# Kernel tuning notes

Measured on AMD Instinct MI355X. Metric: run time of the kernel, lower is better.

The kernel has to match this reference:

```python
import jax, jax.numpy as jnp
import numpy as np

B, N, C = 64, 1024, 128


def setup_inputs() -> dict:
    key = jax.random.key(0)
    k1, k2, k3, k4, k5, k6 = jax.random.split(key, 6)
    adj_vals = jax.random.uniform(k1, (B, N, N), dtype=jnp.float32)
    mask = jax.random.uniform(k2, (B, N, N)) < 0.1
    adjacent = jnp.where(mask, adj_vals, 0.0)
    annotations = jax.random.normal(k3, (B, N, C), dtype=jnp.float32)
    # GraphConvolution bias, shape (1,1,C)
    gc_bias = jax.random.normal(k4, (1, 1, C), dtype=jnp.float32) * 0.05
    # Keras GRU params (reset_after=True default): kernel (C,3C), recurrent (C,3C), bias (2,3C)
    kernel = jax.random.normal(k5, (C, 3 * C), dtype=jnp.float32) / np.sqrt(C)
    recurrent_kernel = jax.random.normal(k6, (C, 3 * C), dtype=jnp.float32) / np.sqrt(C)
    gru_bias = jnp.zeros((2, 3 * C), dtype=jnp.float32)
    return {"adjacent": adjacent, "annotations": annotations, "gc_bias": gc_bias,
            "kernel": kernel, "recurrent_kernel": recurrent_kernel, "gru_bias": gru_bias}


def reference(adjacent, annotations, gc_bias, kernel, recurrent_kernel, gru_bias):
    # GraphConvolution: per-graph adj @ annotations, batched, + bias
    v = jnp.einsum('bij,bjc->bic', adjacent, annotations) + gc_bias  # [B,N,C]
    b, n, c = v.shape
    x = v.reshape(-1, c)            # visible states, one GRU step each
    h = annotations.reshape(-1, c)  # initial hidden states
    # single-step Keras GRU (reset_after=True)
    mx = x @ kernel + gru_bias[0]
    mh = h @ recurrent_kernel + gru_bias[1]
    xz, xr, xh = jnp.split(mx, 3, axis=-1)
    hz, hr, hh_in = jnp.split(mh, 3, axis=-1)
    z = jax.nn.sigmoid(xz + hz)
    r = jax.nn.sigmoid(xr + hr)
    hh = jnp.tanh(xh + r * hh_in)
    out = z * h + (1.0 - z) * hh
    return out.reshape(b, n, c)
```

## Files before the change

### kernel.cpp

```cpp
#include <hip/hip_runtime.h>

typedef unsigned short ushort_t;
typedef __attribute__((ext_vector_type(8))) short bf16x8;
typedef __attribute__((ext_vector_type(8))) unsigned short u16x8;
typedef __attribute__((ext_vector_type(4))) float f32x4;

#define B_ 64
#define N_ 1024
#define C_ 128

static __device__ __forceinline__ float bf2f(unsigned short u) {
  union { unsigned int i; float f; } v; v.i = ((unsigned int)u) << 16; return v.f;
}
static __device__ __forceinline__ unsigned short f2bf(float f) {
  union { float f; unsigned int i; } v; v.f = f;
  unsigned int i = v.i;
  return (unsigned short)((i + 0x7FFFu + ((i >> 16) & 1u)) >> 16);
}
static __device__ __forceinline__ void split1(float x, ushort_t& h, ushort_t& l) {
  union { float f; unsigned int i; } u; u.f = x;
  h = (ushort_t)(u.i >> 16);
  union { unsigned int i; float f; } t; t.i = u.i & 0xFFFF0000u;
  union { float f; unsigned int i; } w; w.f = x - t.f;
  l = (ushort_t)(w.i >> 16);
}
static __device__ __forceinline__ bf16x8 as_bf(u16x8 v) {
  union { u16x8 u; bf16x8 b; } x; x.u = v; return x.b;
}
static __device__ __forceinline__ void gload_lds16(const void* g, void* l) {
  __builtin_amdgcn_global_load_lds((const __attribute__((address_space(1))) void*)g,
                                   (__attribute__((address_space(3))) void*)l,
                                   16, 0, 0);
}

__global__ __launch_bounds__(256) void tsplit(const float* __restrict__ src,
                                              ushort_t* __restrict__ dh,
                                              ushort_t* __restrict__ dl,
                                              int rows, int cols, long sb, long db) {
  __shared__ float tile[64][65];
  const int t = threadIdx.x;
  src += (long)blockIdx.z * sb;
  dh  += (long)blockIdx.z * db;
  dl  += (long)blockIdx.z * db;
  const int r0 = blockIdx.y * 64, c0 = blockIdx.x * 64;
#pragma unroll
  for (int p = 0; p < 4; ++p) {
    int row = p * 16 + (t >> 4), c4 = (t & 15) * 4;
    f32x4 v = *(const f32x4*)(src + (long)(r0 + row) * cols + c0 + c4);
#pragma unroll
    for (int j = 0; j < 4; ++j) tile[row][c4 + j] = v[j];
  }
  __syncthreads();
  const int oc = t >> 2;
#pragma unroll
  for (int p = 0; p < 2; ++p) {
    int ck = (t & 3) + p * 4;
    u16x8 vh, vl;
#pragma unroll
    for (int j = 0; j < 8; ++j) {
      ushort_t hj, lj;
      split1(tile[ck * 8 + j][oc], hj, lj);
      vh[j] = hj; vl[j] = lj;
    }
    long o = (long)(c0 + oc) * rows + r0 + ck * 8;
    *(u16x8*)(dh + o) = vh;
    *(u16x8*)(dl + o) = vl;
  }
}

__global__ __launch_bounds__(256, 2) void gc_gemm(const float* __restrict__ adj,
                                                  const ushort_t* __restrict__ annTh,
                                                  const ushort_t* __restrict__ annTl,
                                                  const float* __restrict__ gcb,
                                                  float* __restrict__ vout) {
  __shared__ __align__(16) ushort_t ldsAh[128 * 64];
  __shared__ __align__(16) ushort_t ldsAl[128 * 64];
  __shared__ __align__(16) ushort_t ldsBh[128 * 64];
  __shared__ __align__(16) ushort_t ldsBl[128 * 64];
  const int tid = threadIdx.x;
  const int w = tid >> 6, lane = tid & 63;
  const int wr = w >> 1, wc = w & 1;
  const int b = blockIdx.x >> 3;
  const int m0 = (blockIdx.x & 7) * 128;

  const float*    adjb = adj   + ((long)b * N_ + m0) * N_;
  const ushort_t* aThb = annTh + (long)b * C_ * N_;
  const ushort_t* aTlb = annTl + (long)b * C_ * N_;

  const int srow8 = lane >> 3;
  const int klog  = ((lane & 7) * 16) ^ (srow8 << 4);
  const int fr = lane & 15;
  const int kg = lane >> 4;

  f32x4 acc[4][4] = {};

  for (int k0 = 0; k0 < N_; k0 += 64) {
#pragma unroll
    for (int jj = 0; jj < 4; ++jj) {
      int j = w * 4 + jj;
      long so = (long)(j * 8 + srow8) * N_ + k0 + (klog >> 1);
      gload_lds16(aThb + so, (void*)&ldsBh[j * 512]);
      gload_lds16(aTlb + so, (void*)&ldsBl[j * 512]);
    }
#pragma unroll
    for (int q = 0; q < 4; ++q) {
      int ch = q * 256 + tid;
      int row = ch >> 3, ce = ch & 7;
      const float* g = adjb + (long)row * N_ + k0 + ce * 8;
      f32x4 a0 = *(const f32x4*)g;
      f32x4 a1 = *(const f32x4*)(g + 4);
      u16x8 vh, vl;
#pragma unroll
      for (int j = 0; j < 4; ++j) {
        ushort_t hj, lj;
        split1(a0[j], hj, lj); vh[j] = hj; vl[j] = lj;
        split1(a1[j], hj, lj); vh[4 + j] = hj; vl[4 + j] = lj;
      }
      int kb = (ce * 16) ^ ((row & 7) << 4);
      *(u16x8*)((char*)ldsAh + row * 128 + kb) = vh;
      *(u16x8*)((char*)ldsAl + row * 128 + kb) = vl;
    }
    __syncthreads();
#pragma unroll
    for (int kk = 0; kk < 2; ++kk) {
      bf16x8 ah[4], al[4], bh[4], bl[4];
#pragma unroll
      for (int mi = 0; mi < 4; ++mi) {
        int row = wr * 64 + mi * 16 + fr;
        int kb = (kk * 64 + kg * 16) ^ ((row & 7) << 4);
        ah[mi] = *(const bf16x8*)((const char*)ldsAh + row * 128 + kb);
        al[mi] = *(const bf16x8*)((const char*)ldsAl + row * 128 + kb);
      }
#pragma unroll
      for (int ni = 0; ni < 4; ++ni) {
        int row = wc * 64 + ni * 16 + fr;
        int kb = (kk * 64 + kg * 16) ^ ((row & 7) << 4);
        bh[ni] = *(const bf16x8*)((const char*)ldsBh + row * 128 + kb);
        bl[ni] = *(const bf16x8*)((const char*)ldsBl + row * 128 + kb);
      }
#pragma unroll
      for (int mi = 0; mi < 4; ++mi)
#pragma unroll
        for (int ni = 0; ni < 4; ++ni) {
          acc[mi][ni] = __builtin_amdgcn_mfma_f32_16x16x32_bf16(ah[mi], bh[ni], acc[mi][ni], 0, 0, 0);
          acc[mi][ni] = __builtin_amdgcn_mfma_f32_16x16x32_bf16(al[mi], bh[ni], acc[mi][ni], 0, 0, 0);
          acc[mi][ni] = __builtin_amdgcn_mfma_f32_16x16x32_bf16(ah[mi], bl[ni], acc[mi][ni], 0, 0, 0);
        }
    }
    __syncthreads();
  }

  const long rowbase = (long)b * N_ + m0 + wr * 64;
#pragma unroll
  for (int ni = 0; ni < 4; ++ni) {
    int col = wc * 64 + ni * 16 + fr;
    float bias = gcb[col];
#pragma unroll
    for (int mi = 0; mi < 4; ++mi)
#pragma unroll
      for (int r = 0; r < 4; ++r)
        vout[(rowbase + mi * 16 + kg * 4 + r) * C_ + col] = acc[mi][ni][r] + bias;
  }
}

#define GATE(G, AK0, AK1, AR0, AR1)                                                         \
  do {                                                                                      \
    const ushort_t* kh_ = kTh + (long)((G) * C_ + cb) * C_;                                 \
    const ushort_t* kl_ = kTl + (long)((G) * C_ + cb) * C_;                                 \
    const ushort_t* rh_ = rTh + (long)((G) * C_ + cb) * C_;                                 \
    bf16x8 KH[4], KL[4], RH[4];                                                             \
    _Pragma("unroll")                                                                       \
    for (int kk = 0; kk < 4; ++kk) {                                                        \
      int o_ = kk * 32 + kg * 8;                                                            \
      KH[kk] = *(const bf16x8*)(kh_ + o_);                                                  \
      KL[kk] = *(const bf16x8*)(kl_ + o_);                                                  \
      RH[kk] = *(const bf16x8*)(rh_ + o_);                                                  \
    }                                                                                       \
    _Pragma("unroll")                                                                       \
    for (int kk = 0; kk < 4; ++kk) {                                                        \
      AK0 = __builtin_amdgcn_mfma_f32_16x16x32_bf16(xh[0][kk], KH[kk], AK0, 0, 0, 0);       \
      AK1 = __builtin_amdgcn_mfma_f32_16x16x32_bf16(xh[1][kk], KH[kk], AK1, 0, 0, 0);       \
      AK0 = __builtin_amdgcn_mfma_f32_16x16x32_bf16(xl[0][kk], KH[kk], AK0, 0, 0, 0);       \
      AK1 = __builtin_amdgcn_mfma_f32_16x16x32_bf16(xl[1][kk], KH[kk], AK1, 0, 0, 0);       \
      AK0 = __builtin_amdgcn_mfma_f32_16x16x32_bf16(xh[0][kk], KL[kk], AK0, 0, 0, 0);       \
      AK1 = __builtin_amdgcn_mfma_f32_16x16x32_bf16(xh[1][kk], KL[kk], AK1, 0, 0, 0);       \
    }                                                                                       \
    _Pragma("unroll")                                                                       \
    for (int kk = 0; kk < 4; ++kk) {                                                        \
      AR0 = __builtin_amdgcn_mfma_f32_16x16x32_bf16(hh[0][kk], RH[kk], AR0, 0, 0, 0);       \
      AR1 = __builtin_amdgcn_mfma_f32_16x16x32_bf16(hh[1][kk], RH[kk], AR1, 0, 0, 0);       \
    }                                                                                       \
  } while (0)

__global__ __launch_bounds__(256, 2) void gru(const float* __restrict__ v,
                                              const float* __restrict__ ann,
                                              const ushort_t* __restrict__ kTh,
                                              const ushort_t* __restrict__ kTl,
                                              const ushort_t* __restrict__ rTh,
                                              const float* __restrict__ gb,
                                              float* __restrict__ out) {
  const int w = threadIdx.x >> 6, lane = threadIdx.x & 63;
  const long m0 = ((long)blockIdx.x * 4 + w) * 32;
  const int fr = lane & 15, kg = lane >> 4;

  bf16x8 xh[2][4], xl[2][4], hh[2][4];
#pragma unroll
  for (int s = 0; s < 2; ++s)
#pragma unroll
    for (int kk = 0; kk < 4; ++kk) {
      long off = (m0 + s * 16 + fr) * (long)C_ + kk * 32 + kg * 8;
      f32x4 x0 = *(const f32x4*)(v + off);
      f32x4 x1 = *(const f32x4*)(v + off + 4);
      u16x8 th, tl;
#pragma unroll
      for (int j = 0; j < 4; ++j) {
        ushort_t hj, lj;
        split1(x0[j], hj, lj); th[j] = hj; tl[j] = lj;
        split1(x1[j], hj, lj); th[4 + j] = hj; tl[4 + j] = lj;
      }
      xh[s][kk] = as_bf(th); xl[s][kk] = as_bf(tl);
      f32x4 h0 = *(const f32x4*)(ann + off);
      f32x4 h1 = *(const f32x4*)(ann + off + 4);
      u16x8 hv;
#pragma unroll
      for (int j = 0; j < 4; ++j) { hv[j] = f2bf(h0[j]); hv[4 + j] = f2bf(h1[j]); }
      hh[s][kk] = as_bf(hv);
    }

#pragma unroll 1
  for (int n = 0; n < 8; ++n) {
    const int cb = n * 16 + fr;
    f32x4 az0 = {}, az1 = {}, ar0 = {}, ar1 = {}, ax0 = {}, ax1 = {}, ah0 = {}, ah1 = {};
    GATE(0, az0, az1, az0, az1);
    GATE(1, ar0, ar1, ar0, ar1);
    GATE(2, ax0, ax1, ah0, ah1);

    const float bz  = gb[cb] + gb[384 + cb];
    const float brr = gb[128 + cb] + gb[384 + 128 + cb];
    const float bxh = gb[256 + cb];
    const float bhi = gb[384 + 256 + cb];
#pragma unroll
    for (int s = 0; s < 2; ++s) {
      const f32x4& az_ = s ? az1 : az0;
      const f32x4& ar_ = s ? ar1 : ar0;
      const f32x4& ax_ = s ? ax1 : ax0;
      const f32x4& ah_ = s ? ah1 : ah0;
#pragma unroll
      for (int r = 0; r < 4; ++r) {
        long row = m0 + s * 16 + kg * 4 + r;
        float hval = ann[row * C_ + cb];
        float zz = 1.f / (1.f + __expf(-(az_[r] + bz)));
        float rr = 1.f / (1.f + __expf(-(ar_[r] + brr)));
        float hpre = ax_[r] + bxh + rr * (ah_[r] + bhi);
        hpre = fminf(fmaxf(hpre, -15.f), 15.f);
        float e2 = __expf(2.f * hpre);
        float th = (e2 - 1.f) / (e2 + 1.f);
        out[row * C_ + cb] = zz * hval + (1.f - zz) * th;
      }
    }
  }
}

extern "C" void kernel_launch(void* const* d_in, const int* in_sizes, int n_in,
                              void* d_out, int out_size, void* d_ws, size_t ws_size,
                              hipStream_t stream) {
  const float* adj = (const float*)d_in[0];
  const float* ann = (const float*)d_in[1];
  const float* gcb = (const float*)d_in[2];
  const float* ker = (const float*)d_in[3];
  const float* rk  = (const float*)d_in[4];
  const float* gb  = (const float*)d_in[5];
  float* out = (float*)d_out;

  char* ws = (char*)d_ws;
  ushort_t* annTh = (ushort_t*)(ws);
  ushort_t* annTl = (ushort_t*)(ws + 16777216);
  ushort_t* kTh   = (ushort_t*)(ws + 33554432);
  ushort_t* kTl   = (ushort_t*)(ws + 33652736);
  ushort_t* rTh   = (ushort_t*)(ws + 33751040);
  ushort_t* rTl   = (ushort_t*)(ws + 33849344);
  float*    v     = (float*)(ws + 33947648);

  hipLaunchKernelGGL(tsplit, dim3(2, 16, 64), dim3(256), 0, stream,
                     ann, annTh, annTl, 1024, 128, (long)1024 * 128, (long)128 * 1024);
  hipLaunchKernelGGL(tsplit, dim3(6, 2, 1), dim3(256), 0, stream,
                     ker, kTh, kTl, 128, 384, 0L, 0L);
  hipLaunchKernelGGL(tsplit, dim3(6, 2, 1), dim3(256), 0, stream,
                     rk, rTh, rTl, 128, 384, 0L, 0L);
  hipLaunchKernelGGL(gc_gemm, dim3(512), dim3(256), 0, stream, adj, annTh, annTl, gcb, v);
  hipLaunchKernelGGL(gru, dim3(512), dim3(256), 0, stream, v, ann, kTh, kTl, rTh, gb, out);
}
```

Baseline: 198.9 us.

## Fuse graph-conv GEMM and GRU into one kernel via LDS staging

After: 165.0 us. 1.21x faster.

```diff
diff --git a/kernel.cpp b/kernel.cpp
--- a/kernel.cpp
+++ b/kernel.cpp
@@ -9,9 +9,6 @@
 #define N_ 1024
 #define C_ 128
 
-static __device__ __forceinline__ float bf2f(unsigned short u) {
-  union { unsigned int i; float f; } v; v.i = ((unsigned int)u) << 16; return v.f;
-}
 static __device__ __forceinline__ unsigned short f2bf(float f) {
   union { float f; unsigned int i; } v; v.f = f;
   unsigned int i = v.i;
@@ -68,20 +65,28 @@
   }
 }
 
-__global__ __launch_bounds__(256, 2) void gc_gemm(const float* __restrict__ adj,
-                                                  const ushort_t* __restrict__ annTh,
-                                                  const ushort_t* __restrict__ annTl,
-                                                  const float* __restrict__ gcb,
-                                                  float* __restrict__ vout) {
-  __shared__ __align__(16) ushort_t ldsAh[128 * 64];
-  __shared__ __align__(16) ushort_t ldsAl[128 * 64];
-  __shared__ __align__(16) ushort_t ldsBh[128 * 64];
-  __shared__ __align__(16) ushort_t ldsBl[128 * 64];
+__global__ __launch_bounds__(256, 2) void gc_gru(const float* __restrict__ adj,
+                                                 const ushort_t* __restrict__ annTh,
+                                                 const ushort_t* __restrict__ annTl,
+                                                 const float* __restrict__ ann,
+                                                 const float* __restrict__ gcb,
+                                                 const ushort_t* __restrict__ kTh,
+                                                 const ushort_t* __restrict__ kTl,
+                                                 const ushort_t* __restrict__ rTh,
+                                                 const float* __restrict__ gb,
+                                                 float* __restrict__ out) {
+  __shared__ __align__(16) float vlds[128 * 132];
+  ushort_t* ldsAh = (ushort_t*)vlds;
+  ushort_t* ldsAl = ldsAh + 128 * 64;
+  ushort_t* ldsBh = ldsAl + 128 * 64;
+  ushort_t* ldsBl = ldsBh + 128 * 64;
+
   const int tid = threadIdx.x;
   const int w = tid >> 6, lane = tid & 63;
   const int wr = w >> 1, wc = w & 1;
-  const int b = blockIdx.x >> 3;
-  const int m0 = (blockIdx.x & 7) * 128;
+  const int swz = (blockIdx.x & 7) * 64 + (blockIdx.x >> 3);
+  const int b = swz >> 3;
+  const int m0 = (swz & 7) * 128;
 
   const float*    adjb = adj   + ((long)b * N_ + m0) * N_;
   const ushort_t* aThb = annTh + (long)b * C_ * N_;
@@ -150,18 +155,47 @@
     __syncthreads();
   }
 
-  const long rowbase = (long)b * N_ + m0 + wr * 64;
 #pragma unroll
   for (int ni = 0; ni < 4; ++ni) {
     int col = wc * 64 + ni * 16 + fr;
     float bias = gcb[col];
 #pragma unroll
-    for (int mi = 0; mi < 4; ++mi)
+    for (int mi = 0; mi < 4; ++mi) {
+      int row = wr * 64 + mi * 16 + kg * 4;
 #pragma unroll
       for (int r = 0; r < 4; ++r)
-        vout[(rowbase + mi * 16 + kg * 4 + r) * C_ + col] = acc[mi][ni][r] + bias;
-  }
-}
+        vlds[(row + r) * 132 + col] = acc[mi][ni][r] + bias;
+    }
+  }
+  __syncthreads();
+
+  const long grow = (long)b * N_ + m0 + w * 32;
+
+  bf16x8 xh[2][4], xl[2][4], hh[2][4];
+#pragma unroll
+  for (int s = 0; s < 2; ++s)
+#pragma unroll
+    for (int kk = 0; kk < 4; ++kk) {
+      int lrow = w * 32 + s * 16 + fr;
+      int k0 = kk * 32 + kg * 8;
+      f32x4 x0 = *(const f32x4*)&vlds[lrow * 132 + k0];
+      f32x4 x1 = *(const f32x4*)&vlds[lrow * 132 + k0 + 4];
+      u16x8 th, tl;
+#pragma unroll
+      for (int j = 0; j < 4; ++j) {
+        ushort_t hj, lj;
+        split1(x0[j], hj, lj); th[j] = hj; tl[j] = lj;
+        split1(x1[j], hj, lj); th[4 + j] = hj; tl[4 + j] = lj;
+      }
+      xh[s][kk] = as_bf(th); xl[s][kk] = as_bf(tl);
+      const float* hrow = ann + (grow + s * 16 + fr) * C_ + k0;
+      f32x4 h0 = *(const f32x4*)hrow;
+      f32x4 h1 = *(const f32x4*)(hrow + 4);
+      u16x8 hv;
+#pragma unroll
+      for (int j = 0; j < 4; ++j) { hv[j] = f2bf(h0[j]); hv[4 + j] = f2bf(h1[j]); }
+      hh[s][kk] = as_bf(hv);
+    }
 
 #define GATE(G, AK0, AK1, AR0, AR1)                                                         \
   do {                                                                                      \
@@ -192,41 +226,6 @@
     }                                                                                       \
   } while (0)
 
-__global__ __launch_bounds__(256, 2) void gru(const float* __restrict__ v,
-                                              const float* __restrict__ ann,
-                                              const ushort_t* __restrict__ kTh,
-                                              const ushort_t* __restrict__ kTl,
-                                              const ushort_t* __restrict__ rTh,
-                                              const float* __restrict__ gb,
-                                              float* __restrict__ out) {
-  const int w = threadIdx.x >> 6, lane = threadIdx.x & 63;
-  const long m0 = ((long)blockIdx.x * 4 + w) * 32;
-  const int fr = lane & 15, kg = lane >> 4;
-
-  bf16x8 xh[2][4], xl[2][4], hh[2][4];
-#pragma unroll
-  for (int s = 0; s < 2; ++s)
-#pragma unroll
-    for (int kk = 0; kk < 4; ++kk) {
-      long off = (m0 + s * 16 + fr) * (long)C_ + kk * 32 + kg * 8;
-      f32x4 x0 = *(const f32x4*)(v + off);
-      f32x4 x1 = *(const f32x4*)(v + off + 4);
-      u16x8 th, tl;
-#pragma unroll
-      for (int j = 0; j < 4; ++j) {
-        ushort_t hj, lj;
-        split1(x0[j], hj, lj); th[j] = hj; tl[j] = lj;
-        split1(x1[j], hj, lj); th[4 + j] = hj; tl[4 + j] = lj;
-      }
-      xh[s][kk] = as_bf(th); xl[s][kk] = as_bf(tl);
-      f32x4 h0 = *(const f32x4*)(ann + off);
-      f32x4 h1 = *(const f32x4*)(ann + off + 4);
-      u16x8 hv;
-#pragma unroll
-      for (int j = 0; j < 4; ++j) { hv[j] = f2bf(h0[j]); hv[4 + j] = f2bf(h1[j]); }
-      hh[s][kk] = as_bf(hv);
-    }
-
 #pragma unroll 1
   for (int n = 0; n < 8; ++n) {
     const int cb = n * 16 + fr;
@@ -247,7 +246,7 @@
       const f32x4& ah_ = s ? ah1 : ah0;
 #pragma unroll
       for (int r = 0; r < 4; ++r) {
-        long row = m0 + s * 16 + kg * 4 + r;
+        long row = grow + s * 16 + kg * 4 + r;
         float hval = ann[row * C_ + cb];
         float zz = 1.f / (1.f + __expf(-(az_[r] + bz)));
         float rr = 1.f / (1.f + __expf(-(ar_[r] + brr)));
@@ -259,6 +258,7 @@
       }
     }
   }
+#undef GATE
 }
 
 extern "C" void kernel_launch(void* const* d_in, const int* in_sizes, int n_in,
@@ -279,7 +279,6 @@
   ushort_t* kTl   = (ushort_t*)(ws + 33652736);
   ushort_t* rTh   = (ushort_t*)(ws + 33751040);
   ushort_t* rTl   = (ushort_t*)(ws + 33849344);
-  float*    v     = (float*)(ws + 33947648);
 
   hipLaunchKernelGGL(tsplit, dim3(2, 16, 64), dim3(256), 0, stream,
                      ann, annTh, annTl, 1024, 128, (long)1024 * 128, (long)128 * 1024);
@@ -287,6 +286,6 @@
                      ker, kTh, kTl, 128, 384, 0L, 0L);
   hipLaunchKernelGGL(tsplit, dim3(6, 2, 1), dim3(256), 0, stream,
                      rk, rTh, rTl, 128, 384, 0L, 0L);
-  hipLaunchKernelGGL(gc_gemm, dim3(512), dim3(256), 0, stream, adj, annTh, annTl, gcb, v);
-  hipLaunchKernelGGL(gru, dim3(512), dim3(256), 0, stream, v, ann, kTh, kTl, rTh, gb, out);
-}
+  hipLaunchKernelGGL(gc_gru, dim3(512), dim3(256), 0, stream,
+                     adj, annTh, annTl, ann, gcb, kTh, kTl, rTh, gb, out);
+}
```

## Software-pipeline GRU weight loads and remap gc_gemm block order across XCDs

Applied to the files above, without the earlier changes.

After: 203.6 us. +2.4%, slower.

```diff
diff --git a/kernel.cpp b/kernel.cpp
--- a/kernel.cpp
+++ b/kernel.cpp
@@ -9,9 +9,6 @@
 #define N_ 1024
 #define C_ 128
 
-static __device__ __forceinline__ float bf2f(unsigned short u) {
-  union { unsigned int i; float f; } v; v.i = ((unsigned int)u) << 16; return v.f;
-}
 static __device__ __forceinline__ unsigned short f2bf(float f) {
   union { float f; unsigned int i; } v; v.f = f;
   unsigned int i = v.i;
@@ -80,8 +77,9 @@
   const int tid = threadIdx.x;
   const int w = tid >> 6, lane = tid & 63;
   const int wr = w >> 1, wc = w & 1;
-  const int b = blockIdx.x >> 3;
-  const int m0 = (blockIdx.x & 7) * 128;
+  const int swz = (blockIdx.x & 7) * 64 + (blockIdx.x >> 3);
+  const int b = swz >> 3;
+  const int m0 = (swz & 7) * 128;
 
   const float*    adjb = adj   + ((long)b * N_ + m0) * N_;
   const ushort_t* aThb = annTh + (long)b * C_ * N_;
@@ -162,35 +160,6 @@
         vout[(rowbase + mi * 16 + kg * 4 + r) * C_ + col] = acc[mi][ni][r] + bias;
   }
 }
-
-#define GATE(G, AK0, AK1, AR0, AR1)                                                         \
-  do {                                                                                      \
-    const ushort_t* kh_ = kTh + (long)((G) * C_ + cb) * C_;                                 \
-    const ushort_t* kl_ = kTl + (long)((G) * C_ + cb) * C_;                                 \
-    const ushort_t* rh_ = rTh + (long)((G) * C_ + cb) * C_;                                 \
-    bf16x8 KH[4], KL[4], RH[4];                                                             \
-    _Pragma("unroll")                                                                       \
-    for (int kk = 0; kk < 4; ++kk) {                                                        \
-      int o_ = kk * 32 + kg * 8;                                                            \
-      KH[kk] = *(const bf16x8*)(kh_ + o_);                                                  \
-      KL[kk] = *(const bf16x8*)(kl_ + o_);                                                  \
-      RH[kk] = *(const bf16x8*)(rh_ + o_);                                                  \
-    }                                                                                       \
-    _Pragma("unroll")                                                                       \
-    for (int kk = 0; kk < 4; ++kk) {                                                        \
-      AK0 = __builtin_amdgcn_mfma_f32_16x16x32_bf16(xh[0][kk], KH[kk], AK0, 0, 0, 0);       \
-      AK1 = __builtin_amdgcn_mfma_f32_16x16x32_bf16(xh[1][kk], KH[kk], AK1, 0, 0, 0);       \
-      AK0 = __builtin_amdgcn_mfma_f32_16x16x32_bf16(xl[0][kk], KH[kk], AK0, 0, 0, 0);       \
-      AK1 = __builtin_amdgcn_mfma_f32_16x16x32_bf16(xl[1][kk], KH[kk], AK1, 0, 0, 0);       \
-      AK0 = __builtin_amdgcn_mfma_f32_16x16x32_bf16(xh[0][kk], KL[kk], AK0, 0, 0, 0);       \
-      AK1 = __builtin_amdgcn_mfma_f32_16x16x32_bf16(xh[1][kk], KL[kk], AK1, 0, 0, 0);       \
-    }                                                                                       \
-    _Pragma("unroll")                                                                       \
-    for (int kk = 0; kk < 4; ++kk) {                                                        \
-      AR0 = __builtin_amdgcn_mfma_f32_16x16x32_bf16(hh[0][kk], RH[kk], AR0, 0, 0, 0);       \
-      AR1 = __builtin_amdgcn_mfma_f32_16x16x32_bf16(hh[1][kk], RH[kk], AR1, 0, 0, 0);       \
-    }                                                                                       \
-  } while (0)
 
 __global__ __launch_bounds__(256, 2) void gru(const float* __restrict__ v,
                                               const float* __restrict__ ann,
@@ -227,38 +196,109 @@
       hh[s][kk] = as_bf(hv);
     }
 
+  bf16x8 W0K[4], W0L[4], W0R[4], W1K[4], W1L[4], W1R[4];
+  float HV0[8], HV1[8];
+
+#define LOADW(WK, WL, WR, NN, GG)                                              \
+  {                                                                            \
+    const ushort_t* kh_ = kTh + (long)((GG) * C_ + (NN) * 16 + fr) * C_;       \
+    const ushort_t* kl_ = kTl + (long)((GG) * C_ + (NN) * 16 + fr) * C_;       \
+    const ushort_t* rh_ = rTh + (long)((GG) * C_ + (NN) * 16 + fr) * C_;       \
+    _Pragma("unroll")                                                          \
+    for (int kk = 0; kk < 4; ++kk) {                                           \
+      int o_ = kk * 32 + kg * 8;                                               \
+      WK[kk] = *(const bf16x8*)(kh_ + o_);                                     \
+      WL[kk] = *(const bf16x8*)(kl_ + o_);                                     \
+      WR[kk] = *(const bf16x8*)(rh_ + o_);                                     \
+    }                                                                          \
+  }
+
+#define LOADHV(HV, NN)                                                         \
+  _Pragma("unroll")                                                            \
+  for (int s = 0; s < 2; ++s)                                                  \
+    _Pragma("unroll")                                                          \
+    for (int r = 0; r < 4; ++r)                                                \
+      HV[s * 4 + r] = ann[(m0 + s * 16 + kg * 4 + r) * (long)C_ + (NN) * 16 + fr];
+
+#define MATH(WK, WL, WR, AK0, AK1, AR0, AR1)                                   \
+  {                                                                            \
+    _Pragma("unroll")                                                          \
+    for (int kk = 0; kk < 4; ++kk) {                                           \
+      AK0 = __builtin_amdgcn_mfma_f32_16x16x32_bf16(xh[0][kk], WK[kk], AK0, 0, 0, 0); \
+      AK1 = __builtin_amdgcn_mfma_f32_16x16x32_bf16(xh[1][kk], WK[kk], AK1, 0, 0, 0); \
+      AK0 = __builtin_amdgcn_mfma_f32_16x16x32_bf16(xl[0][kk], WK[kk], AK0, 0, 0, 0); \
+      AK1 = __builtin_amdgcn_mfma_f32_16x16x32_bf16(xl[1][kk], WK[kk], AK1, 0, 0, 0); \
+      AK0 = __builtin_amdgcn_mfma_f32_16x16x32_bf16(xh[0][kk], WL[kk], AK0, 0, 0, 0); \
+      AK1 = __builtin_amdgcn_mfma_f32_16x16x32_bf16(xh[1][kk], WL[kk], AK1, 0, 0, 0); \
+    }                                                                          \
+    _Pragma("unroll")                                                          \
+    for (int kk = 0; kk < 4; ++kk) {                                           \
+      AR0 = __builtin_amdgcn_mfma_f32_16x16x32_bf16(hh[0][kk], WR[kk], AR0, 0, 0, 0); \
+      AR1 = __builtin_amdgcn_mfma_f32_16x16x32_bf16(hh[1][kk], WR[kk], AR1, 0, 0, 0); \
+    }                                                                          \
+  }
+
+#define EPILOGUE(NN, HV)                                                       \
+  {                                                                            \
+    const int cb = (NN) * 16 + fr;                                             \
+    const float bz  = gb[cb] + gb[384 + cb];                                   \
+    const float brr = gb[128 + cb] + gb[384 + 128 + cb];                       \
+    const float bxh = gb[256 + cb];                                            \
+    const float bhi = gb[384 + 256 + cb];                                      \
+    _Pragma("unroll")                                                          \
+    for (int s = 0; s < 2; ++s) {                                              \
+      const f32x4& az_ = s ? az1 : az0;                                        \
+      const f32x4& ar_ = s ? ar1 : ar0;                                        \
+      const f32x4& ax_ = s ? ax1 : ax0;                                        \
+      const f32x4& ah_ = s ? ah1 : ah0;                                        \
+      _Pragma("unroll")                                                        \
+      for (int r = 0; r < 4; ++r) {                                            \
+        long row = m0 + s * 16 + kg * 4 + r;                                   \
+        float hval = HV[s * 4 + r];                                            \
+        float zz = 1.f / (1.f + __expf(-(az_[r] + bz)));                       \
+        float rr = 1.f / (1.f + __expf(-(ar_[r] + brr)));                      \
+        float hpre = ax_[r] + bxh + rr * (ah_[r] + bhi);                       \
+        hpre = fminf(fmaxf(hpre, -15.f), 15.f);                                \
+        float e2 = __expf(2.f * hpre);                                         \
+        float th = (e2 - 1.f) / (e2 + 1.f);                                    \
+        out[row * C_ + cb] = zz * hval + (1.f - zz) * th;                      \
+      }                                                                        \
+    }                                                                          \
+  }
+
+  LOADW(W0K, W0L, W0R, 0, 0)
+  LOADHV(HV0, 0)
+
 #pragma unroll 1
-  for (int n = 0; n < 8; ++n) {
-    const int cb = n * 16 + fr;
-    f32x4 az0 = {}, az1 = {}, ar0 = {}, ar1 = {}, ax0 = {}, ax1 = {}, ah0 = {}, ah1 = {};
-    GATE(0, az0, az1, az0, az1);
-    GATE(1, ar0, ar1, ar0, ar1);
-    GATE(2, ax0, ax1, ah0, ah1);
-
-    const float bz  = gb[cb] + gb[384 + cb];
-    const float brr = gb[128 + cb] + gb[384 + 128 + cb];
-    const float bxh = gb[256 + cb];
-    const float bhi = gb[384 + 256 + cb];
-#pragma unroll
-    for (int s = 0; s < 2; ++s) {
-      const f32x4& az_ = s ? az1 : az0;
-      const f32x4& ar_ = s ? ar1 : ar0;
-      const f32x4& ax_ = s ? ax1 : ax0;
-      const f32x4& ah_ = s ? ah1 : ah0;
-#pragma unroll
-      for (int r = 0; r < 4; ++r) {
-        long row = m0 + s * 16 + kg * 4 + r;
-        float hval = ann[row * C_ + cb];
-        float zz = 1.f / (1.f + __expf(-(az_[r] + bz)));
-        float rr = 1.f / (1.f + __expf(-(ar_[r] + brr)));
-        float hpre = ax_[r] + bxh + rr * (ah_[r] + bhi);
-        hpre = fminf(fmaxf(hpre, -15.f), 15.f);
-        float e2 = __expf(2.f * hpre);
-        float th = (e2 - 1.f) / (e2 + 1.f);
-        out[row * C_ + cb] = zz * hval + (1.f - zz) * th;
-      }
-    }
-  }
+  for (int n = 0; n < 8; n += 2) {
+    {
+      f32x4 az0 = {}, az1 = {}, ar0 = {}, ar1 = {}, ax0 = {}, ax1 = {}, ah0 = {}, ah1 = {};
+      LOADW(W1K, W1L, W1R, n, 1)
+      MATH(W0K, W0L, W0R, az0, az1, az0, az1)
+      LOADW(W0K, W0L, W0R, n, 2)
+      MATH(W1K, W1L, W1R, ar0, ar1, ar0, ar1)
+      LOADW(W1K, W1L, W1R, n + 1, 0)
+      LOADHV(HV1, n + 1)
+      MATH(W0K, W0L, W0R, ax0, ax1, ah0, ah1)
+      EPILOGUE(n, HV0)
+    }
+    {
+      f32x4 az0 = {}, az1 = {}, ar0 = {}, ar1 = {}, ax0 = {}, ax1 = {}, ah0 = {}, ah1 = {};
+      LOADW(W0K, W0L, W0R, n + 1, 1)
+      MATH(W1K, W1L, W1R, az0, az1, az0, az1)
+      LOADW(W1K, W1L, W1R, n + 1, 2)
+      MATH(W0K, W0L, W0R, ar0, ar1, ar0, ar1)
+      const int nn2 = (n + 2 < 8) ? (n + 2) : 0;
+      LOADW(W0K, W0L, W0R, nn2, 0)
+      LOADHV(HV0, nn2)
+      MATH(W1K, W1L, W1R, ax0, ax1, ah0, ah1)
+      EPILOGUE(n + 1, HV1)
+    }
+  }
+#undef LOADW
+#undef LOADHV
+#undef MATH
+#undef EPILOGUE
 }
 
 extern "C" void kernel_launch(void* const* d_in, const int* in_sizes, int n_in,
@@ -279,7 +319,7 @@
   ushort_t* kTl   = (ushort_t*)(ws + 33652736);
   ushort_t* rTh   = (ushort_t*)(ws + 33751040);
   ushort_t* rTl   = (ushort_t*)(ws + 33849344);
-  float*    v     = (float*)(ws + 33947648);
+  float*    vbuf  = (float*)(ws + 33947648);
 
   hipLaunchKernelGGL(tsplit, dim3(2, 16, 64), dim3(256), 0, stream,
                      ann, annTh, annTl, 1024, 128, (long)1024 * 128, (long)128 * 1024);
@@ -287,6 +327,8 @@
                      ker, kTh, kTl, 128, 384, 0L, 0L);
   hipLaunchKernelGGL(tsplit, dim3(6, 2, 1), dim3(256), 0, stream,
                      rk, rTh, rTl, 128, 384, 0L, 0L);
-  hipLaunchKernelGGL(gc_gemm, dim3(512), dim3(256), 0, stream, adj, annTh, annTl, gcb, v);
-  hipLaunchKernelGGL(gru, dim3(512), dim3(256), 0, stream, v, ann, kTh, kTl, rTh, gb, out);
-}
+  hipLaunchKernelGGL(gc_gemm, dim3(512), dim3(256), 0, stream,
+                     adj, annTh, annTl, gcb, vbuf);
+  hipLaunchKernelGGL(gru, dim3(512), dim3(256), 0, stream,
+                     vbuf, ann, kTh, kTl, rTh, gb, out);
+}
```
